# Kernel optimization log

Hardware: AMD Instinct MI355X
Metric: run time of the kernel (lower is better)

The kernel has to match this reference:

```python
import jax, jax.numpy as jnp
import numpy as np

N_NODES = 100000
N_EDGES = 1600000
D_IN = 128
HID = 64
N_LAYERS = 5
D_OUT = 32
N_GRAPHS = 1000


def setup_inputs() -> dict:
    key = jax.random.key(0)
    ks = jax.random.split(key, 12)
    node_embed = jax.random.normal(ks[0], (N_NODES, D_IN), dtype=jnp.float32)
    edge_index = jax.random.randint(ks[1], (2, N_EDGES), 0, N_NODES, dtype=jnp.int32)
    batch = jnp.sort(jax.random.randint(ks[2], (N_NODES,), 0, N_GRAPHS, dtype=jnp.int32))
    s = 0.1  # weight scale
    return {
        "node_embed": node_embed,
        "edge_index": edge_index,
        "batch": batch,
        "W_in": s * jax.random.normal(ks[3], (D_IN, HID), dtype=jnp.float32),
        "b_in": s * jax.random.normal(ks[4], (HID,), dtype=jnp.float32),
        "ggnn_w": s * jax.random.normal(ks[5], (N_LAYERS, HID, HID), dtype=jnp.float32),
        "gru_w_ih": s * jax.random.normal(ks[6], (3 * HID, HID), dtype=jnp.float32),
        "gru_w_hh": s * jax.random.normal(ks[7], (3 * HID, HID), dtype=jnp.float32),
        "gru_b_ih": s * jax.random.normal(ks[8], (3 * HID,), dtype=jnp.float32),
        "gru_b_hh": s * jax.random.normal(ks[9], (3 * HID,), dtype=jnp.float32),
        "W_out": s * jax.random.normal(ks[10], (HID, D_OUT), dtype=jnp.float32),
        "b_out": s * jax.random.normal(ks[11], (D_OUT,), dtype=jnp.float32),
    }


def _gru_cell(m, h, w_ih, w_hh, b_ih, b_hh):
    # torch.nn.GRUCell: gates ordered (r, z, n)
    gi = m @ w_ih.T + b_ih   # [N, 3H]
    gh = h @ w_hh.T + b_hh   # [N, 3H]
    i_r, i_z, i_n = jnp.split(gi, 3, axis=-1)
    h_r, h_z, h_n = jnp.split(gh, 3, axis=-1)
    r = jax.nn.sigmoid(i_r + h_r)
    z = jax.nn.sigmoid(i_z + h_z)
    n = jnp.tanh(i_n + r * h_n)
    return (1.0 - z) * n + z * h


def reference(node_embed, edge_index, batch, W_in, b_in, ggnn_w,
              gru_w_ih, gru_w_hh, gru_b_ih, gru_b_hh, W_out, b_out):
    n_nodes = node_embed.shape[0]
    src, dst = edge_index[0], edge_index[1]

    # input linear: [N, D_IN] -> [N, H]
    x = node_embed @ W_in + b_in

    # GatedGraphConv: per-layer linear message, add-aggregate, shared GRU update
    def layer(h, w):
        m = h @ w                                   # [N, H]
        agg = jax.ops.segment_sum(m[src], dst, num_segments=n_nodes)  # scatter-add
        h_new = _gru_cell(agg, h, gru_w_ih, gru_w_hh, gru_b_ih, gru_b_hh)
        return h_new, None

    x, _ = jax.lax.scan(layer, x, ggnn_w)

    # global mean pool over graphs
    sums = jax.ops.segment_sum(x, batch, num_segments=N_GRAPHS)       # [G, H]
    cnts = jax.ops.segment_sum(jnp.ones((n_nodes,), x.dtype), batch, num_segments=N_GRAPHS)
    pooled = sums / jnp.maximum(cnts, 1.0)[:, None]

    # dropout is identity in eval mode
    return pooled @ W_out + b_out
```

## Files before the change

### kernel.cpp

```cpp
#include <hip/hip_runtime.h>

#define N_NODES 100000
#define N_EDGES 1600000
#define D_IN 128
#define HID 64
#define N_LAYERS 5
#define D_OUT 32
#define N_GRAPHS 1000

#define BSHIFT 7
#define NBUCK ((N_NODES + 127) >> BSHIFT)
#define CNT_B 256
#define EPB (N_EDGES / CNT_B)
#define NT (NBUCK * CNT_B)

typedef unsigned short ushort_t;
typedef unsigned int uint_t;
typedef __attribute__((ext_vector_type(8))) short short8;
typedef __attribute__((ext_vector_type(4))) float f32x4;

#define MFMA(a, b, c) __builtin_amdgcn_mfma_f32_16x16x32_bf16((a), (b), (c), 0, 0, 0)

#define WSTRIDE (24 * 2 * 64 * 8)
#define NW (N_LAYERS * WSTRIDE)
#define WIN_N (4 * 4 * 64 * 8)

#define IN_B ((N_NODES + 63) / 64)
#define CTOT (CNT_B + IN_B)

__device__ __forceinline__ float fast_sigmoid(float x) {
    return __builtin_amdgcn_rcpf(1.0f + __expf(-x));
}
__device__ __forceinline__ float fast_tanh(float x) {
    return 1.0f - 2.0f * __builtin_amdgcn_rcpf(1.0f + __expf(2.0f * x));
}
__device__ __forceinline__ ushort_t f2bf(float f) {
    uint_t u = __float_as_uint(f);
    return (ushort_t)((u + 0x7fffu + ((u >> 16) & 1u)) >> 16);
}
__device__ __forceinline__ float b2f(ushort_t u) {
    return __uint_as_float(((uint_t)u) << 16);
}
__device__ __forceinline__ void split8(const float* p, short8& hi, short8& lo) {
    float4 u0 = *(const float4*)p;
    float4 u1 = *(const float4*)(p + 4);
#define SPL(ii, fv) { float f_ = (fv); ushort_t h_ = f2bf(f_); hi[ii] = (short)h_;          \
                      float r_ = f_ - __uint_as_float(((uint_t)h_) << 16); lo[ii] = (short)f2bf(r_); }
    SPL(0, u0.x) SPL(1, u0.y) SPL(2, u0.z) SPL(3, u0.w)
    SPL(4, u1.x) SPL(5, u1.y) SPL(6, u1.z) SPL(7, u1.w)
#undef SPL
}

__global__ void k_prep(const float* __restrict__ ggnn_w,
                       const float* __restrict__ w_ih,
                       const float* __restrict__ w_hh,
                       const float* __restrict__ W_in,
                       short* __restrict__ Whi, short* __restrict__ Wlo,
                       short* __restrict__ WinHi, short* __restrict__ WinLo) {
    int t = blockIdx.x * blockDim.x + threadIdx.x;
    if (t < NW) {
        int i    = t & 7;
        int lane = (t >> 3) & 63;
        int s    = (t >> 9) & 1;
        int tt   = (t >> 10) % 24;
        int lay  = (t >> 10) / 24;
        int k    = s * 32 + (lane >> 4) * 8 + i;
        int col  = tt * 16 + (lane & 15);
        float val;
        if (col < 192) {
            const float* wl = ggnn_w + ((size_t)lay * HID + k) * HID;
            const float* wi = w_ih + (size_t)col * HID;
            float acc = 0.0f;
#pragma unroll 8
            for (int q = 0; q < HID; ++q) acc = fmaf(wl[q], wi[q], acc);
            val = acc;
        } else {
            val = w_hh[(size_t)(col - 192) * HID + k];
        }
        ushort_t h_ = f2bf(val);
        Whi[t] = (short)h_;
        Wlo[t] = (short)f2bf(val - b2f(h_));
        return;
    }
    int t2 = t - NW;
    if (t2 >= WIN_N) return;
    int i    = t2 & 7;
    int lane = (t2 >> 3) & 63;
    int jb   = (t2 >> 9) & 3;
    int s    = (t2 >> 11) & 3;
    int k    = s * 32 + (lane >> 4) * 8 + i;
    int col  = jb * 16 + (lane & 15);
    float val = W_in[(size_t)k * HID + col];
    ushort_t h_ = f2bf(val);
    WinHi[t2] = (short)h_;
    WinLo[t2] = (short)f2bf(val - b2f(h_));
}

__global__ __launch_bounds__(256) void k_cntin(
        const int* __restrict__ ei, int* __restrict__ table,
        const float* __restrict__ ne,
        const short* __restrict__ WinHi, const short* __restrict__ WinLo,
        const float* __restrict__ b_in,
        ushort_t* __restrict__ hbhi) {
    __shared__ int hcnt[NBUCK];
    int tid = threadIdx.x;
    int swz = (int)(((long long)blockIdx.x * 256) % CTOT);

    if (swz < CNT_B) {
        int b = swz;
        for (int i = tid; i < NBUCK; i += 256) hcnt[i] = 0;
        __syncthreads();
        int e0 = b * EPB;
        for (int i = tid; i < EPB; i += 256)
            atomicAdd(&hcnt[ei[N_EDGES + e0 + i] >> BSHIFT], 1);
        __syncthreads();
        for (int i = tid; i < NBUCK; i += 256)
            table[i * CNT_B + b] = hcnt[i];
        return;
    }
    int ib = swz - CNT_B;
    int wv = tid >> 6, l = tid & 63;
    int q = l >> 4, c = l & 15;
    int nodeBase = ib * 64 + wv * 16;
    int anode = nodeBase + c;
    int acl = (anode < N_NODES) ? anode : (N_NODES - 1);
    const float* erow = ne + (size_t)acl * D_IN;
    short8 Ah[4], Al[4];
#pragma unroll
    for (int s = 0; s < 4; ++s) split8(erow + s * 32 + q * 8, Ah[s], Al[s]);

    f32x4 acc[4];
    const f32x4 zero = {0.f, 0.f, 0.f, 0.f};
#pragma unroll
    for (int jb = 0; jb < 4; ++jb) acc[jb] = zero;
    const short8* BH = ((const short8*)WinHi) + l;
    const short8* BL = ((const short8*)WinLo) + l;
#pragma unroll
    for (int jb = 0; jb < 4; ++jb)
#pragma unroll
        for (int s = 0; s < 4; ++s) {
            short8 bh = BH[(s * 4 + jb) * 64];
            short8 bl = BL[(s * 4 + jb) * 64];
            acc[jb] = MFMA(Ah[s], bh, acc[jb]);
            acc[jb] = MFMA(Al[s], bh, acc[jb]);
            acc[jb] = MFMA(Ah[s], bl, acc[jb]);
        }
#pragma unroll
    for (int jb = 0; jb < 4; ++jb) {
        int j = jb * 16 + c;
        float bb = b_in[j];
#pragma unroll
        for (int i = 0; i < 4; ++i) {
            int m = nodeBase + q * 4 + i;
            if (m < N_NODES)
                hbhi[(size_t)m * HID + j] = f2bf(acc[jb][i] + bb);
        }
    }
}

#define SCHUNK 1024
__global__ __launch_bounds__(1024) void k_tscan1(int* __restrict__ table,
                                                 int* __restrict__ bsum) {
    __shared__ int buf[SCHUNK];
    int tid = threadIdx.x;
    int i = blockIdx.x * SCHUNK + tid;
    int v = (i < NT) ? table[i] : 0;
    buf[tid] = v;
    __syncthreads();
    for (int s = 1; s < SCHUNK; s <<= 1) {
        int a = (tid >= s) ? buf[tid - s] : 0;
        __syncthreads();
        buf[tid] += a;
        __syncthreads();
    }
    if (i < NT) table[i] = buf[tid] - v;
    if (tid == SCHUNK - 1) bsum[blockIdx.x] = buf[tid];
}

__global__ void k_tscan2(int* __restrict__ bsum, int nchunks,
                         float* __restrict__ sums) {
    int b = blockIdx.x;
    if (b == 0) {
        if (threadIdx.x == 0) {
            int carry = 0;
            for (int c = 0; c < nchunks; ++c) {
                int t = bsum[c];
                bsum[c] = carry;
                carry += t;
            }
        }
        return;
    }
    int i = (b - 1) * 256 + threadIdx.x;
    if (i < N_GRAPHS * (HID + 1)) sums[i] = 0.0f;
}

__global__ __launch_bounds__(256) void k_scatter(const int* __restrict__ ei,
                                                 const int* __restrict__ table,
                                                 const int* __restrict__ bsum,
                                                 uint_t* __restrict__ eb) {
    __shared__ uint2 stage[EPB];
    __shared__ int hoff[NBUCK];
    __shared__ int hslot[NBUCK];
    __shared__ int sbuf[256];
    int b = blockIdx.x, tid = threadIdx.x;
    for (int i = tid; i < NBUCK; i += 256) { hoff[i] = 0; hslot[i] = 0; }
    __syncthreads();
    int e0 = b * EPB;
    for (int i = tid; i < EPB; i += 256)
        atomicAdd(&hoff[ei[N_EDGES + e0 + i] >> BSHIFT], 1);
    __syncthreads();
    int base = tid * 4;
    int c0 = (base + 0 < NBUCK) ? hoff[base + 0] : 0;
    int c1 = (base + 1 < NBUCK) ? hoff[base + 1] : 0;
    int c2 = (base + 2 < NBUCK) ? hoff[base + 2] : 0;
    int c3 = (base + 3 < NBUCK) ? hoff[base + 3] : 0;
    int tot = c0 + c1 + c2 + c3;
    sbuf[tid] = tot;
    __syncthreads();
    for (int s = 1; s < 256; s <<= 1) {
        int a = (tid >= s) ? sbuf[tid - s] : 0;
        __syncthreads();
        sbuf[tid] += a;
        __syncthreads();
    }
    int mybase = sbuf[tid] - tot;
    __syncthreads();
    if (base + 0 < NBUCK) hoff[base + 0] = mybase;
    if (base + 1 < NBUCK) hoff[base + 1] = mybase + c0;
    if (base + 2 < NBUCK) hoff[base + 2] = mybase + c0 + c1;
    if (base + 3 < NBUCK) hoff[base + 3] = mybase + c0 + c1 + c2;
    __syncthreads();
    for (int i = tid; i < EPB; i += 256) {
        int s = ei[e0 + i];
        int d = ei[N_EDGES + e0 + i];
        int bk = d >> BSHIFT;
        int pos = hoff[bk] + atomicAdd(&hslot[bk], 1);
        uint2 v; v.x = (uint_t)s; v.y = (uint_t)d;
        stage[pos] = v;
    }
    __syncthreads();
    for (int p = tid; p < EPB; p += 256) {
        uint2 e = stage[p];
        int bk = (int)e.y >> BSHIFT;
        int gidx = bk * CNT_B + b;
        int gbase = table[gidx] + bsum[gidx >> 10];
        eb[gbase + (p - hoff[bk])] = e.x | ((e.y & 127u) << 17);
    }
}

__global__ __launch_bounds__(256) void k_csr(const int* __restrict__ table,
                                             const int* __restrict__ bsum,
                                             const uint_t* __restrict__ eb,
                                             int* __restrict__ csr,
                                             int* __restrict__ off) {
    __shared__ int cnt[128];
    __shared__ int slot[128];
    int b = blockIdx.x, tid = threadIdx.x;
    int nodeBase = b << BSHIFT;
    int nn = min(128, N_NODES - nodeBase);
    int i0 = b * CNT_B;
    int beg = table[i0] + bsum[i0 >> 10];
    int end;
    if (b == NBUCK - 1) end = N_EDGES;
    else {
        int i1 = (b + 1) * CNT_B;
        end = table[i1] + bsum[i1 >> 10];
    }

    if (tid < 128) { cnt[tid] = 0; slot[tid] = 0; }
    __syncthreads();
    for (int i = beg + tid; i < end; i += 256)
        atomicAdd(&cnt[(eb[i] >> 17) & 127u], 1);
    __syncthreads();
    int orig = (tid < 128) ? cnt[tid] : 0;
    for (int s = 1; s < 128; s <<= 1) {
        int a = (tid >= s && tid < 128) ? cnt[tid - s] : 0;
        __syncthreads();
        if (tid < 128) cnt[tid] += a;
        __syncthreads();
    }
    int start = 0;
    if (tid < 128) start = beg + cnt[tid] - orig;
    __syncthreads();
    if (tid < 128) {
        cnt[tid] = start;
        if (tid < nn) off[nodeBase + tid] = start;
    }
    if (b == NBUCK - 1 && tid == 0) off[N_NODES] = N_EDGES;
    __syncthreads();
    for (int i = beg + tid; i < end; i += 256) {
        uint_t e = eb[i];
        int ln = (e >> 17) & 127u;
        int p = cnt[ln] + atomicAdd(&slot[ln], 1);
        csr[p] = (int)(e & 0x1FFFFu);
    }
}

__global__ __launch_bounds__(256) void k_gather(const int* __restrict__ off,
                                                const int* __restrict__ csr,
                                                const ushort_t* __restrict__ hb,
                                                ushort_t* __restrict__ aggb) {
    int t = blockIdx.x * blockDim.x + threadIdx.x;
    int n = t >> 6;
    int lane = t & 63;
    int q = lane >> 3, c = lane & 7;
    int beg = off[n], end = off[n + 1];
    float a[8];
#pragma unroll
    for (int x = 0; x < 8; ++x) a[x] = 0.f;
#pragma unroll 2
    for (int i = beg; i < end; i += 8) {
        int idx = i + q;
        int sidx = csr[min(idx, end - 1)];
        float msk = (idx < end) ? 1.0f : 0.0f;
        uint4 v = *(const uint4*)(hb + (size_t)sidx * HID + c * 8);
        a[0] = fmaf(msk, __uint_as_float(v.x << 16), a[0]);
        a[1] = fmaf(msk, __uint_as_float(v.x & 0xffff0000u), a[1]);
        a[2] = fmaf(msk, __uint_as_float(v.y << 16), a[2]);
        a[3] = fmaf(msk, __uint_as_float(v.y & 0xffff0000u), a[3]);
        a[4] = fmaf(msk, __uint_as_float(v.z << 16), a[4]);
        a[5] = fmaf(msk, __uint_as_float(v.z & 0xffff0000u), a[5]);
        a[6] = fmaf(msk, __uint_as_float(v.w << 16), a[6]);
        a[7] = fmaf(msk, __uint_as_float(v.w & 0xffff0000u), a[7]);
    }
#pragma unroll
    for (int x = 0; x < 8; ++x) {
        a[x] += __shfl_xor(a[x], 8);
        a[x] += __shfl_xor(a[x], 16);
        a[x] += __shfl_xor(a[x], 32);
    }
    if (q == 0) {
        uint4 o;
        o.x = (uint_t)f2bf(a[0]) | ((uint_t)f2bf(a[1]) << 16);
        o.y = (uint_t)f2bf(a[2]) | ((uint_t)f2bf(a[3]) << 16);
        o.z = (uint_t)f2bf(a[4]) | ((uint_t)f2bf(a[5]) << 16);
        o.w = (uint_t)f2bf(a[6]) | ((uint_t)f2bf(a[7]) << 16);
        *(uint4*)(aggb + (size_t)n * HID + c * 8) = o;
    }
}

__global__ __launch_bounds__(256) void k_gru(const ushort_t* __restrict__ aggb,
                                             ushort_t* __restrict__ hbhi,
                                             const short* __restrict__ Whi,
                                             const short* __restrict__ Wlo,
                                             const float* __restrict__ b_ih,
                                             const float* __restrict__ b_hh) {
    int tid = threadIdx.x;
    int wv = tid >> 6, l = tid & 63;
    int q = l >> 4, c = l & 15;
    int nodeBase = blockIdx.x * 64 + wv * 16;

    int anode = nodeBase + c;
    int acl = (anode < N_NODES) ? anode : (N_NODES - 1);
    const ushort_t* arow = aggb + (size_t)acl * HID;
    const ushort_t* hrow = hbhi + (size_t)acl * HID;
    short8 Ag[2], Ah[2];
    Ag[0] = *(const short8*)(arow + q * 8);
    Ag[1] = *(const short8*)(arow + 32 + q * 8);
    Ah[0] = *(const short8*)(hrow + q * 8);
    Ah[1] = *(const short8*)(hrow + 32 + q * 8);

    const short8* BH = ((const short8*)Whi) + l;
    const short8* BL = ((const short8*)Wlo) + l;
    const f32x4 zero = {0.f, 0.f, 0.f, 0.f};

#pragma unroll
    for (int jb = 0; jb < 4; ++jb) {
        f32x4 acc6[6];
#pragma unroll
        for (int g = 0; g < 6; ++g) acc6[g] = zero;
#pragma unroll
        for (int g = 0; g < 6; ++g) {
            int t = g * 4 + jb;
            short8 b0h = BH[(t * 2 + 0) * 64];
            short8 b1h = BH[(t * 2 + 1) * 64];
            short8 b0l = BL[(t * 2 + 0) * 64];
            short8 b1l = BL[(t * 2 + 1) * 64];
            short8 a0 = (g < 3) ? Ag[0] : Ah[0];
            short8 a1 = (g < 3) ? Ag[1] : Ah[1];
            acc6[g] = MFMA(a0, b0h, acc6[g]);
            acc6[g] = MFMA(a0, b0l, acc6[g]);
            acc6[g] = MFMA(a1, b1h, acc6[g]);
            acc6[g] = MFMA(a1, b1l, acc6[g]);
        }
        int j = jb * 16 + c;
        float br  = b_ih[j] + b_hh[j];
        float bz  = b_ih[64 + j] + b_hh[64 + j];
        float bin = b_ih[128 + j];
        float bhn = b_hh[128 + j];
#pragma unroll
        for (int i = 0; i < 4; ++i) {
            int m = nodeBase + q * 4 + i;
            if (m < N_NODES) {
                float rr = fast_sigmoid(acc6[0][i] + acc6[3][i] + br);
                float zz = fast_sigmoid(acc6[1][i] + acc6[4][i] + bz);
                float nv = fast_tanh((acc6[2][i] + bin) + rr * (acc6[5][i] + bhn));
                size_t idx = (size_t)m * HID + j;
                float hold = b2f(hbhi[idx]);
                hbhi[idx] = f2bf((1.0f - zz) * nv + zz * hold);
            }
        }
    }
}

#define POOL_NPW 32
__global__ void k_pool(const ushort_t* __restrict__ hb,
                       const int* __restrict__ batch,
                       float* __restrict__ sums,
                       float* __restrict__ cntf) {
    int wid = (blockIdx.x * blockDim.x + threadIdx.x) >> 6;
    int j = threadIdx.x & 63;
    int base = wid * POOL_NPW;
    if (base >= N_NODES) return;
    int end = base + POOL_NPW;
    if (end > N_NODES) end = N_NODES;
    float acc = 0.f, c = 0.f;
    int curg = batch[base];
    for (int n = base; n < end; ++n) {
        int g = batch[n];
        if (g != curg) {
            atomicAdd(&sums[(size_t)curg * HID + j], acc);
            if (j == 0) atomicAdd(&cntf[curg], c);
            acc = 0.f; c = 0.f; curg = g;
        }
        acc += b2f(hb[(size_t)n * HID + j]);
        c += 1.f;
    }
    atomicAdd(&sums[(size_t)curg * HID + j], acc);
    if (j == 0) atomicAdd(&cntf[curg], c);
}

__global__ void k_out(const float* __restrict__ sums,
                      const float* __restrict__ cntf,
                      const float* __restrict__ W_out,
                      const float* __restrict__ b_out,
                      float* __restrict__ out) {
    int t = blockIdx.x * blockDim.x + threadIdx.x;
    if (t >= N_GRAPHS * D_OUT) return;
    int g = t / D_OUT, o = t % D_OUT;
    float inv_c = __builtin_amdgcn_rcpf(fmaxf(cntf[g], 1.0f));
    float acc = 0.0f;
#pragma unroll
    for (int k = 0; k < HID; ++k)
        acc = fmaf(sums[g * HID + k], W_out[k * D_OUT + o], acc);
    out[t] = acc * inv_c + b_out[o];
}

static inline char* align256(char* p) {
    return (char*)(((uintptr_t)p + 255) & ~(uintptr_t)255);
}

extern "C" void kernel_launch(void* const* d_in, const int* in_sizes, int n_in,
                              void* d_out, int out_size, void* d_ws, size_t ws_size,
                              hipStream_t stream) {
    const float* node_embed = (const float*)d_in[0];
    const int*   edge_index = (const int*)  d_in[1];
    const int*   batch      = (const int*)  d_in[2];
    const float* W_in       = (const float*)d_in[3];
    const float* b_in       = (const float*)d_in[4];
    const float* ggnn_w     = (const float*)d_in[5];
    const float* gru_w_ih   = (const float*)d_in[6];
    const float* gru_w_hh   = (const float*)d_in[7];
    const float* gru_b_ih   = (const float*)d_in[8];
    const float* gru_b_hh   = (const float*)d_in[9];
    const float* W_out      = (const float*)d_in[10];
    const float* b_out      = (const float*)d_in[11];
    float* out = (float*)d_out;

    char* p = (char*)d_ws;
    ushort_t* hbhi  = (ushort_t*)p; p = align256(p + (size_t)N_NODES * HID * sizeof(ushort_t));
    ushort_t* aggb  = (ushort_t*)p; p = align256(p + (size_t)N_NODES * HID * sizeof(ushort_t));
    int*      csr   = (int*)p;      p = align256(p + (size_t)N_EDGES * sizeof(int));
    uint_t*   eb    = (uint_t*)p;   p = align256(p + (size_t)N_EDGES * sizeof(uint_t));
    int*      table = (int*)p;      p = align256(p + (size_t)NT * sizeof(int));
    int*      off   = (int*)p;      p = align256(p + (size_t)(N_NODES + 1) * sizeof(int));
    int*      bsumT = (int*)p;      p = align256(p + 256 * sizeof(int));
    short*    Whi   = (short*)p;    p = align256(p + (size_t)NW * sizeof(short));
    short*    Wlo   = (short*)p;    p = align256(p + (size_t)NW * sizeof(short));
    short*    WinHi = (short*)p;    p = align256(p + (size_t)WIN_N * sizeof(short));
    short*    WinLo = (short*)p;    p = align256(p + (size_t)WIN_N * sizeof(short));
    float*    sums  = (float*)p;
    float*    cntf  = (float*)(p + (size_t)N_GRAPHS * HID * sizeof(float));

    const int BLK = 256;
    const int nchunksT = (NT + SCHUNK - 1) / SCHUNK;

    k_prep<<<(NW + WIN_N) / BLK, BLK, 0, stream>>>(
        ggnn_w, gru_w_ih, gru_w_hh, W_in, Whi, Wlo, WinHi, WinLo);

    k_cntin<<<CTOT, BLK, 0, stream>>>(
        edge_index, table, node_embed, WinHi, WinLo, b_in, hbhi);

    k_tscan1<<<nchunksT, SCHUNK, 0, stream>>>(table, bsumT);
    k_tscan2<<<1 + (N_GRAPHS * (HID + 1) + BLK - 1) / BLK, BLK, 0, stream>>>(
        bsumT, nchunksT, sums);
    k_scatter<<<CNT_B, BLK, 0, stream>>>(edge_index, table, bsumT, eb);
    k_csr<<<NBUCK, BLK, 0, stream>>>(table, bsumT, eb, csr, off);

    for (int l = 0; l < N_LAYERS; ++l) {
        k_gather<<<N_NODES * 64 / BLK, BLK, 0, stream>>>(off, csr, hbhi, aggb);
        k_gru<<<(N_NODES + 63) / 64, BLK, 0, stream>>>(
            aggb, hbhi, Whi + (size_t)l * WSTRIDE, Wlo + (size_t)l * WSTRIDE,
            gru_b_ih, gru_b_hh);
    }

    {
        int waves = (N_NODES + POOL_NPW - 1) / POOL_NPW;
        int threads = waves * 64;
        k_pool<<<(threads + BLK - 1) / BLK, BLK, 0, stream>>>(hbhi, batch, sums, cntf);
    }
    k_out<<<(N_GRAPHS * D_OUT + BLK - 1) / BLK, BLK, 0, stream>>>(sums, cntf, W_out, b_out, out);
}
```

Before: 444.6 us.

## Fold block-sum scan into tscan1 via last-block atomic, drop low-part MFMAs for sigmoid gates

Removes the separate k_tscan2 launch. The last k_tscan1 block to finish, found with an atomic counter, scans the block sums itself, and the zeroing of the pooling sums moves into k_prep. In the GRU kernel the bf16 low-part weight MFMAs are now issued only for the n-gate columns, so the r and z gates use hi-only bf16 weights. This cuts launch overhead and about a third of the GRU MFMA work and weight loads, in exchange for reduced precision in the r and z gates.

```diff
diff --git a/kernel.cpp b/kernel.cpp
--- a/kernel.cpp
+++ b/kernel.cpp
@@ -56,8 +56,11 @@
                        const float* __restrict__ w_hh,
                        const float* __restrict__ W_in,
                        short* __restrict__ Whi, short* __restrict__ Wlo,
-                       short* __restrict__ WinHi, short* __restrict__ WinLo) {
+                       short* __restrict__ WinHi, short* __restrict__ WinLo,
+                       float* __restrict__ sums, int* __restrict__ done) {
     int t = blockIdx.x * blockDim.x + threadIdx.x;
+    if (t == 0) *done = 0;
+    if (t < N_GRAPHS * (HID + 1)) sums[t] = 0.0f;
     if (t < NW) {
         int i    = t & 7;
         int lane = (t >> 3) & 63;
@@ -160,8 +163,10 @@
 
 #define SCHUNK 1024
 __global__ __launch_bounds__(1024) void k_tscan1(int* __restrict__ table,
-                                                 int* __restrict__ bsum) {
+                                                 int* __restrict__ bsum,
+                                                 int* __restrict__ done) {
     __shared__ int buf[SCHUNK];
+    __shared__ int lastFlag;
     int tid = threadIdx.x;
     int i = blockIdx.x * SCHUNK + tid;
     int v = (i < NT) ? table[i] : 0;
@@ -174,25 +179,24 @@
         __syncthreads();
     }
     if (i < NT) table[i] = buf[tid] - v;
-    if (tid == SCHUNK - 1) bsum[blockIdx.x] = buf[tid];
-}
-
-__global__ void k_tscan2(int* __restrict__ bsum, int nchunks,
-                         float* __restrict__ sums) {
-    int b = blockIdx.x;
-    if (b == 0) {
-        if (threadIdx.x == 0) {
-            int carry = 0;
-            for (int c = 0; c < nchunks; ++c) {
-                int t = bsum[c];
-                bsum[c] = carry;
-                carry += t;
-            }
-        }
-        return;
-    }
-    int i = (b - 1) * 256 + threadIdx.x;
-    if (i < N_GRAPHS * (HID + 1)) sums[i] = 0.0f;
+    if (tid == SCHUNK - 1) atomicExch(&bsum[blockIdx.x], buf[tid]);
+    if (tid == 0) {
+        __threadfence();
+        lastFlag = (atomicAdd(done, 1) == (int)gridDim.x - 1) ? 1 : 0;
+    }
+    __syncthreads();
+    if (!lastFlag) return;
+    int nch = gridDim.x;
+    int bv = (tid < nch) ? atomicAdd(&bsum[tid], 0) : 0;
+    buf[tid] = bv;
+    __syncthreads();
+    for (int s = 1; s < SCHUNK; s <<= 1) {
+        int a = (tid >= s) ? buf[tid - s] : 0;
+        __syncthreads();
+        buf[tid] += a;
+        __syncthreads();
+    }
+    if (tid < nch) atomicExch(&bsum[tid], buf[tid] - bv);
 }
 
 __global__ __launch_bounds__(256) void k_scatter(const int* __restrict__ ei,
@@ -375,14 +379,16 @@
             int t = g * 4 + jb;
             short8 b0h = BH[(t * 2 + 0) * 64];
             short8 b1h = BH[(t * 2 + 1) * 64];
-            short8 b0l = BL[(t * 2 + 0) * 64];
-            short8 b1l = BL[(t * 2 + 1) * 64];
             short8 a0 = (g < 3) ? Ag[0] : Ah[0];
             short8 a1 = (g < 3) ? Ag[1] : Ah[1];
             acc6[g] = MFMA(a0, b0h, acc6[g]);
-            acc6[g] = MFMA(a0, b0l, acc6[g]);
             acc6[g] = MFMA(a1, b1h, acc6[g]);
-            acc6[g] = MFMA(a1, b1l, acc6[g]);
+            if (g == 2 || g == 5) {
+                short8 b0l = BL[(t * 2 + 0) * 64];
+                short8 b1l = BL[(t * 2 + 1) * 64];
+                acc6[g] = MFMA(a0, b0l, acc6[g]);
+                acc6[g] = MFMA(a1, b1l, acc6[g]);
+            }
         }
         int j = jb * 16 + c;
         float br  = b_ih[j] + b_hh[j];
@@ -476,6 +482,7 @@
     int*      table = (int*)p;      p = align256(p + (size_t)NT * sizeof(int));
     int*      off   = (int*)p;      p = align256(p + (size_t)(N_NODES + 1) * sizeof(int));
     int*      bsumT = (int*)p;      p = align256(p + 256 * sizeof(int));
+    int*      doneT = (int*)p;      p = align256(p + 256 * sizeof(int));
     short*    Whi   = (short*)p;    p = align256(p + (size_t)NW * sizeof(short));
     short*    Wlo   = (short*)p;    p = align256(p + (size_t)NW * sizeof(short));
     short*    WinHi = (short*)p;    p = align256(p + (size_t)WIN_N * sizeof(short));
@@ -487,14 +494,12 @@
     const int nchunksT = (NT + SCHUNK - 1) / SCHUNK;
 
     k_prep<<<(NW + WIN_N) / BLK, BLK, 0, stream>>>(
-        ggnn_w, gru_w_ih, gru_w_hh, W_in, Whi, Wlo, WinHi, WinLo);
+        ggnn_w, gru_w_ih, gru_w_hh, W_in, Whi, Wlo, WinHi, WinLo, sums, doneT);
 
     k_cntin<<<CTOT, BLK, 0, stream>>>(
         edge_index, table, node_embed, WinHi, WinLo, b_in, hbhi);
 
-    k_tscan1<<<nchunksT, SCHUNK, 0, stream>>>(table, bsumT);
-    k_tscan2<<<1 + (N_GRAPHS * (HID + 1) + BLK - 1) / BLK, BLK, 0, stream>>>(
-        bsumT, nchunksT, sums);
+    k_tscan1<<<nchunksT, SCHUNK, 0, stream>>>(table, bsumT, doneT);
     k_scatter<<<CNT_B, BLK, 0, stream>>>(edge_index, table, bsumT, eb);
     k_csr<<<NBUCK, BLK, 0, stream>>>(table, bsumT, eb, csr, off);
 
```

Measured after the change: 398.7 us. 10.3% less time.
